# Kernel tuning notes

Hardware: AMD Instinct MI355X
Metric: run time of the kernel (lower is better)

Reference implementation:

```python
import jax, jax.numpy as jnp
import numpy as np

N, T, D, H = 6144, 3072, 128, 4
ALPHA = 0.2
NEG = -9e15


def mhgat(x, mask, W, a_src, a_dst, fc_W, fc_b):
    # x: [n, D], mask: [n, n] (0/1), W: [H, D, D], a_src/a_dst: [H, D]
    Wh = jnp.einsum('nd,hde->hne', x, W)                      # [H, n, D]
    f_s = jnp.einsum('hne,he->hn', Wh, a_src)                 # [H, n]
    f_d = jnp.einsum('hne,he->hn', Wh, a_dst)                 # [H, n]
    e = jax.nn.leaky_relu(f_s[:, :, None] + f_d[:, None, :], ALPHA)  # [H, n, n]
    scores = jnp.where(mask[None, :, :] > 0, e, NEG)
    attn = jax.nn.softmax(scores, axis=-1)                    # masked softmax over neighbors
    h = jnp.einsum('hnm,hme->hne', attn, Wh)                  # [H, n, D]
    h = jax.nn.elu(h)                                         # concat=True -> elu per head
    h = jnp.transpose(h, (1, 0, 2)).reshape(x.shape[0], H * h.shape[-1])  # [n, H*D]
    return jax.nn.relu(h @ fc_W + fc_b)                       # fully_connectedLyer = Linear+ReLU


def setup_inputs() -> dict:
    key = jax.random.key(0)
    ks = jax.random.split(key, 20)
    s = 0.05
    return {
        'x': jax.random.normal(ks[0], (N, D), jnp.float32),
        'adj': jax.random.randint(ks[1], (N, N), 0, 2, jnp.int32),
        't_x': jax.random.normal(ks[2], (T, D), jnp.float32),
        't_adj': jax.random.randint(ks[3], (T, T), 0, 2, jnp.int32),
        'tfidf_x': jax.random.uniform(ks[4], (T, N), jnp.float32),
        # concept-graph MHGAT params
        'Wg': jax.random.normal(ks[5], (H, D, D), jnp.float32) * s,
        'ag_src': jax.random.normal(ks[6], (H, D), jnp.float32) * s,
        'ag_dst': jax.random.normal(ks[7], (H, D), jnp.float32) * s,
        'fcg_W': jax.random.normal(ks[8], (H * D, D), jnp.float32) * s,
        'fcg_b': jnp.zeros((D,), jnp.float32),
        # text-graph MHGAT params
        'Wt': jax.random.normal(ks[9], (H, D, D), jnp.float32) * s,
        'at_src': jax.random.normal(ks[10], (H, D), jnp.float32) * s,
        'at_dst': jax.random.normal(ks[11], (H, D), jnp.float32) * s,
        'fct_W': jax.random.normal(ks[12], (H * D, D), jnp.float32) * s,
        'fct_b': jnp.zeros((D,), jnp.float32),
        # fusion fc params
        'fus_W': jax.random.normal(ks[13], (D, D), jnp.float32) * s,
        'fus_b': jnp.zeros((D,), jnp.float32),
    }


def reference(x, adj, t_x, t_adj, tfidf_x,
              Wg, ag_src, ag_dst, fcg_W, fcg_b,
              Wt, at_src, at_dst, fct_W, fct_b,
              fus_W, fus_b):
    concept = mhgat(x, adj, Wg, ag_src, ag_dst, fcg_W, fcg_b)        # [N, D]
    gat_text = mhgat(t_x, t_adj, Wt, at_src, at_dst, fct_W, fct_b)   # [T, D]
    c_text = tfidf_x.T @ gat_text                                    # [N, D]
    z = jax.nn.sigmoid(concept + c_text)
    fusion = z * concept + (1.0 - z) * c_text
    return jax.nn.relu(fusion @ fus_W + fus_b)
```

## Files before the change

kernel.cpp:

```cpp
#include <hip/hip_runtime.h>
#include <hip/hip_bf16.h>
#include <stdint.h>

#define N_  6144
#define T_  3072
#define D_  128
#define H_  4
#define HD_ 512

typedef float f32x4 __attribute__((ext_vector_type(4)));
typedef short s16x8 __attribute__((ext_vector_type(8)));
typedef _Float16 h16x4 __attribute__((ext_vector_type(4)));

#define GLL16(g, s) __builtin_amdgcn_global_load_lds( \
    (const __attribute__((address_space(1))) unsigned int*)(g), \
    (__attribute__((address_space(3))) unsigned int*)(s), 16, 0, 0)

static __device__ __forceinline__ short f2bf(float f) {
  union { __hip_bfloat16 b; short s; } u;
  u.b = __float2bfloat16(f);
  return u.s;
}

__global__ __launch_bounds__(256) void bits2_kernel(const int* __restrict__ a0,
                                                    const int* __restrict__ a1,
                                                    unsigned long long* __restrict__ b0,
                                                    unsigned long long* __restrict__ b1,
                                                    int nw0, int nw1) {
  int lane = threadIdx.x & 63;
  int gw = (blockIdx.x * blockDim.x + threadIdx.x) >> 6;
  int nw = (gridDim.x * blockDim.x) >> 6;
  int total = nw0 + nw1;
  for (int w = gw; w < total; w += nw) {
    const int* src; unsigned long long* dst; long wi;
    if (w < nw0) { src = a0; dst = b0; wi = w; }
    else         { src = a1; dst = b1; wi = w - nw0; }
    int v = src[wi * 64 + lane];
    unsigned long long b = __ballot(v != 0);
    if (lane == 0) dst[wi] = b;
  }
}

__global__ __launch_bounds__(256) void cvt2_kernel(const float* __restrict__ in0,
                                                   short* __restrict__ out0,
                                                   const float* __restrict__ in1,
                                                   short* __restrict__ out1,
                                                   int c0, int c1) {
  int i = blockIdx.x * blockDim.x + threadIdx.x;
  const float* in; short* out; long ii;
  if (i < c0) { in = in0; out = out0; ii = i; }
  else if (i < c0 + c1) { in = in1; out = out1; ii = i - c0; }
  else return;
  float4 v = *(const float4*)(in + ii * 4);
  short4 o;
  o.x = f2bf(v.x); o.y = f2bf(v.y); o.z = f2bf(v.z); o.w = f2bf(v.w);
  *(short4*)(out + ii * 4) = o;
}

__global__ __launch_bounds__(256) void tcvt2_kernel(const float* __restrict__ in0,
                                                    short* __restrict__ out0,
                                                    const float* __restrict__ in1,
                                                    short* __restrict__ out1,
                                                    int R, int C, long sIn, long sOut,
                                                    int zsplit) {
  __shared__ float t[32][33];
  const float* in; short* out;
  int z = blockIdx.z;
  if (z < zsplit) { in = in0 + (long)z * sIn; out = out0 + (long)z * sOut; }
  else            { in = in1 + (long)(z - zsplit) * sIn; out = out1 + (long)(z - zsplit) * sOut; }
  int c0 = blockIdx.x * 32, r0 = blockIdx.y * 32;
  int tx = threadIdx.x, ty = threadIdx.y;
#pragma unroll
  for (int i = 0; i < 4; ++i)
    t[ty + 8 * i][tx] = in[(long)(r0 + ty + 8 * i) * C + c0 + tx];
  __syncthreads();
#pragma unroll
  for (int i = 0; i < 4; ++i)
    out[(long)(c0 + ty + 8 * i) * R + r0 + tx] = f2bf(t[tx][ty + 8 * i]);
}

__global__ __launch_bounds__(256) void fvec_kernel(const float* __restrict__ x,
                                                   const float* __restrict__ W,
                                                   const float* __restrict__ a_s,
                                                   const float* __restrict__ a_d,
                                                   float* __restrict__ fsA,
                                                   float* __restrict__ fdA,
                                                   int n) {
  __shared__ float usl[128], udl[128], asl[128], adl[128];
  long idx = (long)blockIdx.x * 256 + threadIdx.x;
  int h = (int)(idx / n), i = (int)(idx % n);
  int tid = threadIdx.x;
  if (tid < 128) {
    asl[tid] = a_s[h * D_ + tid];
    adl[tid] = a_d[h * D_ + tid];
  }
  __syncthreads();
  {
    int d = tid & 127;
    const float* wr = W + ((long)h * D_ + d) * D_;
    const float* av = (tid < 128) ? asl : adl;
    float s = 0.f;
#pragma unroll 8
    for (int e = 0; e < D_; ++e) s += wr[e] * av[e];
    if (tid < 128) usl[d] = s; else udl[d] = s;
  }
  __syncthreads();
  const float4* xr = (const float4*)(x + (long)i * D_);
  float s = 0.f, t = 0.f;
#pragma unroll 8
  for (int e4 = 0; e4 < 32; ++e4) {
    float4 xv = xr[e4];
    s += xv.x * usl[4 * e4] + xv.y * usl[4 * e4 + 1] + xv.z * usl[4 * e4 + 2] + xv.w * usl[4 * e4 + 3];
    t += xv.x * udl[4 * e4] + xv.y * udl[4 * e4 + 1] + xv.z * udl[4 * e4 + 2] + xv.w * udl[4 * e4 + 3];
  }
  const float L2E = 1.4426950408889634f;
  fsA[idx] = s * L2E;
  fdA[idx] = t * L2E;
}

__global__ __launch_bounds__(256) void gemm_kernel(const short* __restrict__ A,
                                                   const short* __restrict__ BT,
                                                   int K, int lda, int ldb,
                                                   float* __restrict__ outF, short* __restrict__ outB,
                                                   int ldo, int epi,
                                                   long sA, long sBT, long sOut) {
  int bz = blockIdx.z;
  A += bz * sA;
  BT += bz * sBT;
  __shared__ __align__(16) short bs[2][4096];
  int tid = threadIdx.x, w = tid >> 6, l = tid & 63, lm = l & 15, lg = l >> 4;
  int row0 = blockIdx.x * 64 + w * 16;
  int col0 = blockIdx.y * 128;
  const short* arow = A + (long)(row0 + lm) * lda + 8 * lg;
  const short* bsrc = BT + (long)(col0 + 16 * (2 * w) + lm) * ldb + 8 * lg;
  f32x4 acc[8] = {};
  int nt = K / 32;
  s16x8 af = *(const s16x8*)(arow);
  GLL16(bsrc, &bs[0][(2 * w) * 512]);
  GLL16(bsrc + 16 * ldb, &bs[0][(2 * w + 1) * 512]);
  for (int kt = 0; kt < nt; ++kt) {
    int cur = kt & 1, nxt = cur ^ 1;
    int kb = (kt + 1 < nt ? kt + 1 : kt) * 32;
    s16x8 an = *(const s16x8*)(arow + kb);
    asm volatile("s_waitcnt vmcnt(1)" ::: "memory");
    __builtin_amdgcn_sched_barrier(0);
    __builtin_amdgcn_s_barrier();
    __builtin_amdgcn_sched_barrier(0);
#pragma unroll
    for (int f = 0; f < 8; ++f) {
      s16x8 bf = *(const s16x8*)(&bs[cur][f * 512 + l * 8]);
      acc[f] = __builtin_amdgcn_mfma_f32_16x16x32_bf16(af, bf, acc[f], 0, 0, 0);
    }
    if (kt + 1 < nt) {
      GLL16(bsrc + kb, &bs[nxt][(2 * w) * 512]);
      GLL16(bsrc + kb + 16 * ldb, &bs[nxt][(2 * w + 1) * 512]);
    }
    __builtin_amdgcn_sched_barrier(0);
    af = an;
  }
#pragma unroll
  for (int f = 0; f < 8; ++f) {
    int col = col0 + 16 * f + lm;
#pragma unroll
    for (int r = 0; r < 4; ++r) {
      int row = row0 + 4 * lg + r;
      if (epi == 0) outB[bz * sOut + (long)row * ldo + col] = f2bf(acc[f][r]);
      else          outF[bz * sOut + (long)row * ldo + col] = acc[f][r];
    }
  }
}

__global__ __launch_bounds__(256) void reduce_kernel(const float* __restrict__ P,
                                                     int S, long sP,
                                                     const float* __restrict__ bias,
                                                     short* __restrict__ outB,
                                                     int ldo) {
  __shared__ short sm[128][68];
  int tid = threadIdx.x;
  int r0 = blockIdx.x * 64;
#pragma unroll
  for (int k = 0; k < 8; ++k) {
    int e = tid * 4 + k * 1024;
    int row = e >> 7, col = e & 127;
    f32x4 v = {};
    for (int s = 0; s < S; ++s)
      v += *(const f32x4*)(P + (long)s * sP + (long)(r0 + row) * 128 + col);
    const float4 bv = *(const float4*)(bias + col);
    v[0] += bv.x; v[1] += bv.y; v[2] += bv.z; v[3] += bv.w;
#pragma unroll
    for (int q = 0; q < 4; ++q) v[q] = v[q] > 0.f ? v[q] : 0.f;
    sm[col + 0][row] = f2bf(v[0]);
    sm[col + 1][row] = f2bf(v[1]);
    sm[col + 2][row] = f2bf(v[2]);
    sm[col + 3][row] = f2bf(v[3]);
  }
  __syncthreads();
  int d = tid >> 1, seg = tid & 1;
  short* dst = outB + (long)d * ldo + r0 + seg * 32;
#pragma unroll
  for (int q = 0; q < 8; ++q) {
    short4 o;
    o.x = sm[d][seg * 32 + 4 * q + 0];
    o.y = sm[d][seg * 32 + 4 * q + 1];
    o.z = sm[d][seg * 32 + 4 * q + 2];
    o.w = sm[d][seg * 32 + 4 * q + 3];
    *(short4*)(dst + 4 * q) = o;
  }
}

__global__ __launch_bounds__(256) void attn_kernel(const short* __restrict__ WhT,
                                                   const unsigned char* __restrict__ bits,
                                                   const float* __restrict__ fsA,
                                                   const float* __restrict__ fdA,
                                                   _Float16* __restrict__ pacc,
                                                   float* __restrict__ pz,
                                                   int n, int S) {
  int h = blockIdx.y, sp = blockIdx.z;
  int RB = gridDim.x;
  int klen = n / S, k0 = sp * klen;
  const short* whT = WhT + (long)h * D_ * n;
  const float* fa = fdA + (long)h * n;
  __shared__ __align__(16) short bs[2][4096];
  int tid = threadIdx.x, w = tid >> 6, l = tid & 63, lm = l & 15, lg = l >> 4;
  int i0 = blockIdx.x * 128;
  int r0 = i0 + 32 * w + lm;
  int r1 = r0 + 16;
  float fs0 = fsA[(long)h * n + r0];
  float fs1 = fsA[(long)h * n + r1];
  const unsigned char* brow0 = bits + (long)r0 * (n >> 3);
  const unsigned char* brow1 = bits + (long)r1 * (n >> 3);
  const short* bsrc = whT + (long)(16 * (2 * w) + lm) * n + 8 * lg + k0;
  f32x4 acc0[8] = {}, acc1[8] = {};
  f32x4 az0 = {}, az1 = {};
  s16x8 ones;
#pragma unroll
  for (int j = 0; j < 8; ++j) ones[j] = (short)0x3F80;
  const int NEGB = __float_as_int(-1e30f);
  int nt = klen / 32;
  float favA[8], favB[8];
  unsigned m0A, m1A, m0B, m1B;
  *(float4*)(favA)     = *(const float4*)(fa + k0 + 8 * lg);
  *(float4*)(favA + 4) = *(const float4*)(fa + k0 + 8 * lg + 4);
  m0A = (*(const unsigned*)(brow0 + (k0 >> 3))) >> (8 * lg);
  m1A = (*(const unsigned*)(brow1 + (k0 >> 3))) >> (8 * lg);
  GLL16(bsrc, &bs[0][(2 * w) * 512]);
  GLL16(bsrc + 16 * n, &bs[0][(2 * w + 1) * 512]);

#define ATTN_STEP(KT, FAVC, M0C, M1C, FAVN, M0N, M1N)                           \
  {                                                                             \
    int cur = (KT) & 1, nxt = cur ^ 1;                                          \
    int kb = ((KT) + 1 < nt ? (KT) + 1 : (KT)) * 32;                            \
    *(float4*)(FAVN)     = *(const float4*)(fa + k0 + kb + 8 * lg);             \
    *(float4*)(FAVN + 4) = *(const float4*)(fa + k0 + kb + 8 * lg + 4);         \
    M0N = (*(const unsigned*)(brow0 + ((k0 + kb) >> 3))) >> (8 * lg);           \
    M1N = (*(const unsigned*)(brow1 + ((k0 + kb) >> 3))) >> (8 * lg);           \
    union { s16x8 v; unsigned u[4]; } af0, af1;                                 \
    _Pragma("unroll")                                                           \
    for (int jj = 0; jj < 4; ++jj) {                                            \
      float xa = FAVC[2 * jj], xb2 = FAVC[2 * jj + 1];                          \
      int ta = ((int)(M0C << (31 - 2 * jj))) >> 31;                             \
      int tb = ((int)(M0C << (30 - 2 * jj))) >> 31;                             \
      float ua = fs0 + xa, ub = fs0 + xb2;                                      \
      ua = __int_as_float((ta & __float_as_int(ua)) | (~ta & NEGB));            \
      ub = __int_as_float((tb & __float_as_int(ub)) | (~tb & NEGB));            \
      float pa = __builtin_amdgcn_exp2f(fmaxf(ua, 0.2f * ua));                  \
      float pb = __builtin_amdgcn_exp2f(fmaxf(ub, 0.2f * ub));                  \
      af0.u[jj] = __builtin_amdgcn_perm(__float_as_uint(pb) + 0x8000u,          \
                                        __float_as_uint(pa) + 0x8000u, 0x07060302); \
      ta = ((int)(M1C << (31 - 2 * jj))) >> 31;                                 \
      tb = ((int)(M1C << (30 - 2 * jj))) >> 31;                                 \
      ua = fs1 + xa; ub = fs1 + xb2;                                            \
      ua = __int_as_float((ta & __float_as_int(ua)) | (~ta & NEGB));            \
      ub = __int_as_float((tb & __float_as_int(ub)) | (~tb & NEGB));            \
      pa = __builtin_amdgcn_exp2f(fmaxf(ua, 0.2f * ua));                        \
      pb = __builtin_amdgcn_exp2f(fmaxf(ub, 0.2f * ub));                        \
      af1.u[jj] = __builtin_amdgcn_perm(__float_as_uint(pb) + 0x8000u,          \
                                        __float_as_uint(pa) + 0x8000u, 0x07060302); \
    }                                                                           \
    asm volatile("s_waitcnt vmcnt(4)" ::: "memory");                            \
    __builtin_amdgcn_sched_barrier(0);                                          \
    __builtin_amdgcn_s_barrier();                                               \
    __builtin_amdgcn_sched_barrier(0);                                          \
    _Pragma("unroll")                                                           \
    for (int f = 0; f < 8; ++f) {                                               \
      s16x8 bf = *(const s16x8*)(&bs[cur][f * 512 + l * 8]);                    \
      acc0[f] = __builtin_amdgcn_mfma_f32_16x16x32_bf16(af0.v, bf, acc0[f], 0, 0, 0); \
      acc1[f] = __builtin_amdgcn_mfma_f32_16x16x32_bf16(af1.v, bf, acc1[f], 0, 0, 0); \
    }                                                                           \
    az0 = __builtin_amdgcn_mfma_f32_16x16x32_bf16(af0.v, ones, az0, 0, 0, 0);   \
    az1 = __builtin_amdgcn_mfma_f32_16x16x32_bf16(af1.v, ones, az1, 0, 0, 0);   \
    if ((KT) + 1 < nt) {                                                        \
      GLL16(bsrc + kb, &bs[nxt][(2 * w) * 512]);                                \
      GLL16(bsrc + kb + 16 * n, &bs[nxt][(2 * w + 1) * 512]);                   \
    }                                                                           \
    __builtin_amdgcn_sched_barrier(0);                                          \
  }

  for (int kt = 0; kt < nt; kt += 2) {
    ATTN_STEP(kt,     favA, m0A, m1A, favB, m0B, m1B);
    ATTN_STEP(kt + 1, favB, m0B, m1B, favA, m0A, m1A);
  }
#undef ATTN_STEP

  long base = (long)(h * RB + blockIdx.x) * S + sp;
  if (lm == 0) {
#pragma unroll
    for (int r = 0; r < 4; ++r) {
      pz[base * 128 + 32 * w + 4 * lg + r] = az0[r];
      pz[base * 128 + 32 * w + 16 + 4 * lg + r] = az1[r];
    }
  }
  long pb = base * 16384;
#pragma unroll
  for (int f = 0; f < 8; ++f)
#pragma unroll
    for (int r = 0; r < 4; ++r) {
      pacc[pb + (long)(32 * w + 4 * lg + r) * 128 + 16 * f + lm] = (_Float16)acc0[f][r];
      pacc[pb + (long)(32 * w + 16 + 4 * lg + r) * 128 + 16 * f + lm] = (_Float16)acc1[f][r];
    }
}

__global__ __launch_bounds__(256) void attn_combine_kernel(const _Float16* __restrict__ pacc,
                                                           const float* __restrict__ pz,
                                                           short* __restrict__ hcat,
                                                           int S) {
  int h = blockIdx.y, rb = blockIdx.x;
  int RB = gridDim.x;
  long base = (long)(h * RB + rb) * S;
  __shared__ float zl[128];
  int tid = threadIdx.x;
  if (tid < 128) {
    float zv = 0.f;
    for (int s = 0; s < S; ++s) zv += pz[(base + s) * 128 + tid];
    zl[tid] = 1.f / zv;
  }
  __syncthreads();
  int i0 = rb * 128;
#pragma unroll
  for (int k = 0; k < 16; ++k) {
    int e = tid * 4 + k * 1024;
    int row = e >> 7, col = e & 127;
    f32x4 v = {};
    for (int s = 0; s < S; ++s) {
      h16x4 hv = *(const h16x4*)(pacc + (base + s) * 16384 + e);
      v[0] += (float)hv[0]; v[1] += (float)hv[1];
      v[2] += (float)hv[2]; v[3] += (float)hv[3];
    }
    float iz = zl[row];
    short4 o;
    float t;
    t = v[0] * iz; o.x = f2bf(t > 0.f ? t : __expf(t) - 1.f);
    t = v[1] * iz; o.y = f2bf(t > 0.f ? t : __expf(t) - 1.f);
    t = v[2] * iz; o.z = f2bf(t > 0.f ? t : __expf(t) - 1.f);
    t = v[3] * iz; o.w = f2bf(t > 0.f ? t : __expf(t) - 1.f);
    *(short4*)(hcat + (long)(i0 + row) * HD_ + h * D_ + col) = o;
  }
}

__global__ __launch_bounds__(256) void fusion_kernel(const float* __restrict__ fcPg,
                                                     int Sf, long sPg,
                                                     const float* __restrict__ fcg_b,
                                                     const float* __restrict__ ctextP,
                                                     int Sc, long sCt,
                                                     const short* __restrict__ fusT,
                                                     const float* __restrict__ fus_b,
                                                     float* __restrict__ out) {
  __shared__ __align__(16) short als[64 * 136];
  int tid = threadIdx.x;
  int r0 = blockIdx.x * 64;
#pragma unroll
  for (int it = 0; it < 8; ++it) {
    int e = it * 1024 + tid * 4;
    int r = e >> 7, c = e & 127;
    f32x4 cv = {};
    for (int s = 0; s < Sf; ++s)
      cv += *(const f32x4*)(fcPg + (long)s * sPg + (long)(r0 + r) * D_ + c);
    const float4 bv = *(const float4*)(fcg_b + c);
    cv[0] += bv.x; cv[1] += bv.y; cv[2] += bv.z; cv[3] += bv.w;
#pragma unroll
    for (int q = 0; q < 4; ++q) cv[q] = cv[q] > 0.f ? cv[q] : 0.f;
    f32x4 tv = {};
    for (int s = 0; s < Sc; ++s)
      tv += *(const f32x4*)(ctextP + (long)s * sCt + (long)(r0 + r) * D_ + c);
    short4 o;
    {
      float s0 = cv[0] + tv[0]; float z = 1.f / (1.f + __expf(-s0)); o.x = f2bf(tv[0] + z * (cv[0] - tv[0]));
      s0 = cv[1] + tv[1]; z = 1.f / (1.f + __expf(-s0)); o.y = f2bf(tv[1] + z * (cv[1] - tv[1]));
      s0 = cv[2] + tv[2]; z = 1.f / (1.f + __expf(-s0)); o.z = f2bf(tv[2] + z * (cv[2] - tv[2]));
      s0 = cv[3] + tv[3]; z = 1.f / (1.f + __expf(-s0)); o.w = f2bf(tv[3] + z * (cv[3] - tv[3]));
    }
    *(short4*)(als + (long)r * 136 + c) = o;
  }
  __syncthreads();
  int w = tid >> 6, l = tid & 63, lm = l & 15, lg = l >> 4;
  f32x4 acc[8] = {};
#pragma unroll
  for (int kt = 0; kt < 4; ++kt) {
    int kb = kt * 32;
    s16x8 af = *(const s16x8*)(als + (16 * w + lm) * 136 + kb + 8 * lg);
#pragma unroll
    for (int f = 0; f < 8; ++f) {
      s16x8 bf = *(const s16x8*)(fusT + (long)(16 * f + lm) * D_ + kb + 8 * lg);
      acc[f] = __builtin_amdgcn_mfma_f32_16x16x32_bf16(af, bf, acc[f], 0, 0, 0);
    }
  }
#pragma unroll
  for (int f = 0; f < 8; ++f) {
    int col = 16 * f + lm;
#pragma unroll
    for (int r = 0; r < 4; ++r) {
      float v = acc[f][r] + fus_b[col];
      v = v > 0.f ? v : 0.f;
      out[(long)(r0 + 16 * w + 4 * lg + r) * D_ + col] = v;
    }
  }
}

extern "C" void kernel_launch(void* const* d_in, const int* in_sizes, int n_in,
                              void* d_out, int out_size, void* d_ws, size_t ws_size,
                              hipStream_t stream) {
  (void)in_sizes; (void)n_in; (void)out_size;
  const float* x      = (const float*)d_in[0];
  const int*   adj    = (const int*)d_in[1];
  const float* t_x    = (const float*)d_in[2];
  const int*   t_adj  = (const int*)d_in[3];
  const float* tfidf  = (const float*)d_in[4];
  const float* Wg     = (const float*)d_in[5];
  const float* ag_src = (const float*)d_in[6];
  const float* ag_dst = (const float*)d_in[7];
  const float* fcg_W  = (const float*)d_in[8];
  const float* fcg_b  = (const float*)d_in[9];
  const float* Wt     = (const float*)d_in[10];
  const float* at_src = (const float*)d_in[11];
  const float* at_dst = (const float*)d_in[12];
  const float* fct_W  = (const float*)d_in[13];
  const float* fct_b  = (const float*)d_in[14];
  const float* fus_W  = (const float*)d_in[15];
  const float* fus_b  = (const float*)d_in[16];
  float* out = (float*)d_out;

  char* ws = (char*)d_ws;
  size_t off = 0;
  auto alloc = [&](size_t bytes) -> char* {
    char* p = ws + off;
    off = (off + bytes + 255) & ~(size_t)255;
    return p;
  };
  unsigned long long* bitsG = (unsigned long long*)alloc((size_t)N_ * N_ / 8);
  unsigned long long* bitsT = (unsigned long long*)alloc((size_t)T_ * T_ / 8);
  short* xb     = (short*)alloc((size_t)N_ * D_ * 2);
  short* txb    = (short*)alloc((size_t)T_ * D_ * 2);
  short* WgT    = (short*)alloc((size_t)H_ * D_ * D_ * 2);
  short* WtT    = (short*)alloc((size_t)H_ * D_ * D_ * 2);
  short* fcgT   = (short*)alloc((size_t)HD_ * D_ * 2);
  short* fctT   = (short*)alloc((size_t)HD_ * D_ * 2);
  short* fusT   = (short*)alloc((size_t)D_ * D_ * 2);
  short* tfidfT = (short*)alloc((size_t)N_ * T_ * 2);
  short* WhTg   = (short*)alloc((size_t)H_ * D_ * N_ * 2);
  short* WhTt   = (short*)alloc((size_t)H_ * D_ * T_ * 2);
  float* fsAg = (float*)alloc((size_t)H_ * N_ * 4);
  float* fdAg = (float*)alloc((size_t)H_ * N_ * 4);
  float* fsAt = (float*)alloc((size_t)H_ * T_ * 4);
  float* fdAt = (float*)alloc((size_t)H_ * T_ * 4);
  short* hcatG = (short*)alloc((size_t)N_ * HD_ * 2);
  short* hcatT = (short*)alloc((size_t)T_ * HD_ * 2);
  short* gatT  = (short*)alloc((size_t)D_ * T_ * 2);

  const int RBg = N_ / 128, RBt = T_ / 128;
  const size_t paccG1 = (size_t)H_ * RBg * 16384 * 2;
  const size_t paccT1 = (size_t)H_ * RBt * 16384 * 2;
  const size_t pzG1   = (size_t)H_ * RBg * 128 * 4;
  const size_t pzT1   = (size_t)H_ * RBt * 128 * 4;
  const size_t fcPg1  = (size_t)N_ * D_ * 4;
  const size_t fcPt1  = (size_t)T_ * D_ * 4;
  const size_t ctp1   = (size_t)N_ * D_ * 4;
  size_t rem = (ws_size > off + (1 << 20)) ? (ws_size - off - (1 << 20)) : 0;
  int Sg = 2, St = 2, Sf = 1, Sc = 1;
  size_t needFull = 8 * (paccG1 + pzG1) + 8 * (paccT1 + pzT1) + 4 * fcPg1 + 4 * fcPt1 + 4 * ctp1;
  size_t needMid  = 4 * (paccG1 + pzG1) + 4 * (paccT1 + pzT1) + 2 * fcPg1 + 2 * fcPt1 + 2 * ctp1;
  if (rem >= needFull)      { Sg = 8; St = 8; Sf = 4; Sc = 4; }
  else if (rem >= needMid)  { Sg = 4; St = 4; Sf = 2; Sc = 2; }
  _Float16* paccG = (_Float16*)alloc(Sg * paccG1);
  float* pzG   = (float*)alloc(Sg * pzG1);
  _Float16* paccT = (_Float16*)alloc(St * paccT1);
  float* pzT   = (float*)alloc(St * pzT1);
  float* fcPg  = (float*)alloc(Sf * fcPg1);
  float* fcPt  = (float*)alloc(Sf * fcPt1);
  float* ctextP = (float*)alloc(Sc * ctp1);

  bits2_kernel<<<dim3(1536), dim3(256), 0, stream>>>(adj, t_adj, bitsG, bitsT,
                                                     N_ * N_ / 64, T_ * T_ / 64);
  cvt2_kernel<<<dim3((N_ + T_) * D_ / 1024), dim3(256), 0, stream>>>(
      x, xb, t_x, txb, N_ * D_ / 4, T_ * D_ / 4);
  tcvt2_kernel<<<dim3(4, 4, 8), dim3(32, 8), 0, stream>>>(
      Wg, WgT, Wt, WtT, D_, D_, (long)D_ * D_, (long)D_ * D_, 4);
  tcvt2_kernel<<<dim3(4, 16, 2), dim3(32, 8), 0, stream>>>(
      fcg_W, fcgT, fct_W, fctT, HD_, D_, 0, 0, 1);
  tcvt2_kernel<<<dim3(4, 4, 1), dim3(32, 8), 0, stream>>>(
      fus_W, fusT, fus_W, fusT, D_, D_, 0, 0, 1);
  tcvt2_kernel<<<dim3(N_ / 32, T_ / 32, 1), dim3(32, 8), 0, stream>>>(
      tfidf, tfidfT, tfidf, tfidfT, T_, N_, 0, 0, 1);
  fvec_kernel<<<dim3(H_ * N_ / 256), dim3(256), 0, stream>>>(x, Wg, ag_src, ag_dst, fsAg, fdAg, N_);
  fvec_kernel<<<dim3(H_ * T_ / 256), dim3(256), 0, stream>>>(t_x, Wt, at_src, at_dst, fsAt, fdAt, T_);

  gemm_kernel<<<dim3(2, N_ / 128, H_), dim3(256), 0, stream>>>(
      WgT, xb, D_, D_, D_, nullptr, WhTg, N_, 0, (long)D_ * D_, 0, (long)D_ * N_);
  gemm_kernel<<<dim3(2, T_ / 128, H_), dim3(256), 0, stream>>>(
      WtT, txb, D_, D_, D_, nullptr, WhTt, T_, 0, (long)D_ * D_, 0, (long)D_ * T_);

  attn_kernel<<<dim3(RBg, H_, Sg), dim3(256), 0, stream>>>(
      WhTg, (const unsigned char*)bitsG, fsAg, fdAg, paccG, pzG, N_, Sg);
  attn_combine_kernel<<<dim3(RBg, H_), dim3(256), 0, stream>>>(paccG, pzG, hcatG, Sg);
  attn_kernel<<<dim3(RBt, H_, St), dim3(256), 0, stream>>>(
      WhTt, (const unsigned char*)bitsT, fsAt, fdAt, paccT, pzT, T_, St);
  attn_combine_kernel<<<dim3(RBt, H_), dim3(256), 0, stream>>>(paccT, pzT, hcatT, St);

  gemm_kernel<<<dim3(N_ / 64, 1, Sf), dim3(256), 0, stream>>>(
      hcatG, fcgT, HD_ / Sf, HD_, HD_, fcPg, nullptr, D_, 3,
      (long)(HD_ / Sf), (long)(HD_ / Sf), (long)N_ * D_);
  gemm_kernel<<<dim3(T_ / 64, 1, Sf), dim3(256), 0, stream>>>(
      hcatT, fctT, HD_ / Sf, HD_, HD_, fcPt, nullptr, D_, 3,
      (long)(HD_ / Sf), (long)(HD_ / Sf), (long)T_ * D_);
  reduce_kernel<<<dim3(T_ / 64), dim3(256), 0, stream>>>(
      fcPt, Sf, (long)T_ * D_, fct_b, gatT, T_);

  gemm_kernel<<<dim3(N_ / 64, 1, Sc), dim3(256), 0, stream>>>(
      tfidfT, gatT, T_ / Sc, T_, T_, ctextP, nullptr, D_, 3,
      (long)(T_ / Sc), (long)(T_ / Sc), (long)N_ * D_);

  fusion_kernel<<<dim3(N_ / 64), dim3(256), 0, stream>>>(
      fcPg, Sf, (long)N_ * D_, fcg_b, ctextP, Sc, (long)N_ * D_, fusT, fus_b, out);
}
```

Measured before the change: 414.0 us.

## Factor attention exponentials into per-node precomputed terms and batch mask bit packing

```diff
diff --git a/kernel.cpp b/kernel.cpp
--- a/kernel.cpp
+++ b/kernel.cpp
@@ -22,7 +22,7 @@
   return u.s;
 }
 
-__global__ __launch_bounds__(256) void bits2_kernel(const int* __restrict__ a0,
+__global__ __launch_bounds__(256) void bits8_kernel(const int* __restrict__ a0,
                                                     const int* __restrict__ a1,
                                                     unsigned long long* __restrict__ b0,
                                                     unsigned long long* __restrict__ b1,
@@ -30,14 +30,26 @@
   int lane = threadIdx.x & 63;
   int gw = (blockIdx.x * blockDim.x + threadIdx.x) >> 6;
   int nw = (gridDim.x * blockDim.x) >> 6;
-  int total = nw0 + nw1;
-  for (int w = gw; w < total; w += nw) {
+  int total8 = (nw0 + nw1) >> 3;
+  for (int g = gw; g < total8; g += nw) {
+    int w = g * 8;
     const int* src; unsigned long long* dst; long wi;
     if (w < nw0) { src = a0; dst = b0; wi = w; }
     else         { src = a1; dst = b1; wi = w - nw0; }
-    int v = src[wi * 64 + lane];
-    unsigned long long b = __ballot(v != 0);
-    if (lane == 0) dst[wi] = b;
+    int v[8];
+#pragma unroll
+    for (int j = 0; j < 8; ++j) v[j] = src[(wi + j) * 64 + lane];
+    unsigned long long bb[8];
+#pragma unroll
+    for (int j = 0; j < 8; ++j) bb[j] = __ballot(v[j] != 0);
+    if (lane == 0) {
+      ulonglong2 s01 = {bb[0], bb[1]}, s23 = {bb[2], bb[3]};
+      ulonglong2 s45 = {bb[4], bb[5]}, s67 = {bb[6], bb[7]};
+      *(ulonglong2*)(dst + wi + 0) = s01;
+      *(ulonglong2*)(dst + wi + 2) = s23;
+      *(ulonglong2*)(dst + wi + 4) = s45;
+      *(ulonglong2*)(dst + wi + 6) = s67;
+    }
   }
 }
 
@@ -83,8 +95,9 @@
                                                    const float* __restrict__ W,
                                                    const float* __restrict__ a_s,
                                                    const float* __restrict__ a_d,
-                                                   float* __restrict__ fsA,
-                                                   float* __restrict__ fdA,
+                                                   float* __restrict__ ea, float* __restrict__ ec,
+                                                   float* __restrict__ inv,
+                                                   float* __restrict__ eb, float* __restrict__ ed,
                                                    int n) {
   __shared__ float usl[128], udl[128], asl[128], adl[128];
   long idx = (long)blockIdx.x * 256 + threadIdx.x;
@@ -114,8 +127,12 @@
     t += xv.x * udl[4 * e4] + xv.y * udl[4 * e4 + 1] + xv.z * udl[4 * e4 + 2] + xv.w * udl[4 * e4 + 3];
   }
   const float L2E = 1.4426950408889634f;
-  fsA[idx] = s * L2E;
-  fdA[idx] = t * L2E;
+  float fs = s * L2E, fd = t * L2E;
+  ea[idx]  = exp2f(fs);
+  ec[idx]  = exp2f(0.2f * fs);
+  inv[idx] = exp2f(-fs);
+  eb[idx]  = exp2f(fd);
+  ed[idx]  = exp2f(0.2f * fd);
 }
 
 __global__ __launch_bounds__(256) void gemm_kernel(const short* __restrict__ A,
@@ -210,8 +227,11 @@
 
 __global__ __launch_bounds__(256) void attn_kernel(const short* __restrict__ WhT,
                                                    const unsigned char* __restrict__ bits,
-                                                   const float* __restrict__ fsA,
-                                                   const float* __restrict__ fdA,
+                                                   const float* __restrict__ eaA,
+                                                   const float* __restrict__ ecA,
+                                                   const float* __restrict__ invA,
+                                                   const float* __restrict__ ebA,
+                                                   const float* __restrict__ edA,
                                                    _Float16* __restrict__ pacc,
                                                    float* __restrict__ pz,
                                                    int n, int S) {
@@ -219,14 +239,16 @@
   int RB = gridDim.x;
   int klen = n / S, k0 = sp * klen;
   const short* whT = WhT + (long)h * D_ * n;
-  const float* fa = fdA + (long)h * n;
+  const float* ebp = ebA + (long)h * n;
+  const float* edp = edA + (long)h * n;
   __shared__ __align__(16) short bs[2][4096];
   int tid = threadIdx.x, w = tid >> 6, l = tid & 63, lm = l & 15, lg = l >> 4;
   int i0 = blockIdx.x * 128;
   int r0 = i0 + 32 * w + lm;
   int r1 = r0 + 16;
-  float fs0 = fsA[(long)h * n + r0];
-  float fs1 = fsA[(long)h * n + r1];
+  float ea0 = eaA[(long)h * n + r0], ea1 = eaA[(long)h * n + r1];
+  float ec0 = ecA[(long)h * n + r0], ec1 = ecA[(long)h * n + r1];
+  float iv0 = invA[(long)h * n + r0], iv1 = invA[(long)h * n + r1];
   const unsigned char* brow0 = bits + (long)r0 * (n >> 3);
   const unsigned char* brow1 = bits + (long)r1 * (n >> 3);
   const short* bsrc = whT + (long)(16 * (2 * w) + lm) * n + 8 * lg + k0;
@@ -235,49 +257,53 @@
   s16x8 ones;
 #pragma unroll
   for (int j = 0; j < 8; ++j) ones[j] = (short)0x3F80;
-  const int NEGB = __float_as_int(-1e30f);
   int nt = klen / 32;
-  float favA[8], favB[8];
+  float ebR[8], edR[8], ebS[8], edS[8];
   unsigned m0A, m1A, m0B, m1B;
-  *(float4*)(favA)     = *(const float4*)(fa + k0 + 8 * lg);
-  *(float4*)(favA + 4) = *(const float4*)(fa + k0 + 8 * lg + 4);
+  *(float4*)(ebR)     = *(const float4*)(ebp + k0 + 8 * lg);
+  *(float4*)(ebR + 4) = *(const float4*)(ebp + k0 + 8 * lg + 4);
+  *(float4*)(edR)     = *(const float4*)(edp + k0 + 8 * lg);
+  *(float4*)(edR + 4) = *(const float4*)(edp + k0 + 8 * lg + 4);
   m0A = (*(const unsigned*)(brow0 + (k0 >> 3))) >> (8 * lg);
   m1A = (*(const unsigned*)(brow1 + (k0 >> 3))) >> (8 * lg);
   GLL16(bsrc, &bs[0][(2 * w) * 512]);
   GLL16(bsrc + 16 * n, &bs[0][(2 * w + 1) * 512]);
 
-#define ATTN_STEP(KT, FAVC, M0C, M1C, FAVN, M0N, M1N)                           \
+#define ATTN_STEP(KT, EBC, EDC, M0C, M1C, EBN, EDN, M0N, M1N)                   \
   {                                                                             \
     int cur = (KT) & 1, nxt = cur ^ 1;                                          \
     int kb = ((KT) + 1 < nt ? (KT) + 1 : (KT)) * 32;                            \
-    *(float4*)(FAVN)     = *(const float4*)(fa + k0 + kb + 8 * lg);             \
-    *(float4*)(FAVN + 4) = *(const float4*)(fa + k0 + kb + 8 * lg + 4);         \
+    *(float4*)(EBN)     = *(const float4*)(ebp + k0 + kb + 8 * lg);             \
+    *(float4*)(EBN + 4) = *(const float4*)(ebp + k0 + kb + 8 * lg + 4);         \
+    *(float4*)(EDN)     = *(const float4*)(edp + k0 + kb + 8 * lg);             \
+    *(float4*)(EDN + 4) = *(const float4*)(edp + k0 + kb + 8 * lg + 4);         \
     M0N = (*(const unsigned*)(brow0 + ((k0 + kb) >> 3))) >> (8 * lg);           \
     M1N = (*(const unsigned*)(brow1 + ((k0 + kb) >> 3))) >> (8 * lg);           \
     union { s16x8 v; unsigned u[4]; } af0, af1;                                 \
     _Pragma("unroll")                                                           \
     for (int jj = 0; jj < 4; ++jj) {                                            \
-      float xa = FAVC[2 * jj], xb2 = FAVC[2 * jj + 1];                          \
+      float bva = EBC[2 * jj], bvb = EBC[2 * jj + 1];                           \
+      float dva = EDC[2 * jj], dvb = EDC[2 * jj + 1];                           \
       int ta = ((int)(M0C << (31 - 2 * jj))) >> 31;                             \
       int tb = ((int)(M0C << (30 - 2 * jj))) >> 31;                             \
-      float ua = fs0 + xa, ub = fs0 + xb2;                                      \
-      ua = __int_as_float((ta & __float_as_int(ua)) | (~ta & NEGB));            \
-      ub = __int_as_float((tb & __float_as_int(ub)) | (~tb & NEGB));            \
-      float pa = __builtin_amdgcn_exp2f(fmaxf(ua, 0.2f * ua));                  \
-      float pb = __builtin_amdgcn_exp2f(fmaxf(ub, 0.2f * ub));                  \
+      bool ca = bva > iv0, cb = bvb > iv0;                                      \
+      float pa = (ca ? bva : dva) * (ca ? ea0 : ec0);                           \
+      float pb = (cb ? bvb : dvb) * (cb ? ea0 : ec0);                           \
+      pa = __int_as_float(ta & __float_as_int(pa));                             \
+      pb = __int_as_float(tb & __float_as_int(pb));                             \
       af0.u[jj] = __builtin_amdgcn_perm(__float_as_uint(pb) + 0x8000u,          \
                                         __float_as_uint(pa) + 0x8000u, 0x07060302); \
       ta = ((int)(M1C << (31 - 2 * jj))) >> 31;                                 \
       tb = ((int)(M1C << (30 - 2 * jj))) >> 31;                                 \
-      ua = fs1 + xa; ub = fs1 + xb2;                                            \
-      ua = __int_as_float((ta & __float_as_int(ua)) | (~ta & NEGB));            \
-      ub = __int_as_float((tb & __float_as_int(ub)) | (~tb & NEGB));            \
-      pa = __builtin_amdgcn_exp2f(fmaxf(ua, 0.2f * ua));                        \
-      pb = __builtin_amdgcn_exp2f(fmaxf(ub, 0.2f * ub));                        \
+      ca = bva > iv1; cb = bvb > iv1;                                           \
+      pa = (ca ? bva : dva) * (ca ? ea1 : ec1);                                 \
+      pb = (cb ? bvb : dvb) * (cb ? ea1 : ec1);                                 \
+      pa = __int_as_float(ta & __float_as_int(pa));                             \
+      pb = __int_as_float(tb & __float_as_int(pb));                             \
       af1.u[jj] = __builtin_amdgcn_perm(__float_as_uint(pb) + 0x8000u,          \
                                         __float_as_uint(pa) + 0x8000u, 0x07060302); \
     }                                                                           \
-    asm volatile("s_waitcnt vmcnt(4)" ::: "memory");                            \
+    asm volatile("s_waitcnt vmcnt(6)" ::: "memory");                            \
     __builtin_amdgcn_sched_barrier(0);                                          \
     __builtin_amdgcn_s_barrier();                                               \
     __builtin_amdgcn_sched_barrier(0);                                          \
@@ -297,8 +323,8 @@
   }
 
   for (int kt = 0; kt < nt; kt += 2) {
-    ATTN_STEP(kt,     favA, m0A, m1A, favB, m0B, m1B);
-    ATTN_STEP(kt + 1, favB, m0B, m1B, favA, m0A, m1A);
+    ATTN_STEP(kt,     ebR, edR, m0A, m1A, ebS, edS, m0B, m1B);
+    ATTN_STEP(kt + 1, ebS, edS, m0B, m1B, ebR, edR, m0A, m1A);
   }
 #undef ATTN_STEP
 
@@ -458,10 +484,16 @@
   short* tfidfT = (short*)alloc((size_t)N_ * T_ * 2);
   short* WhTg   = (short*)alloc((size_t)H_ * D_ * N_ * 2);
   short* WhTt   = (short*)alloc((size_t)H_ * D_ * T_ * 2);
-  float* fsAg = (float*)alloc((size_t)H_ * N_ * 4);
-  float* fdAg = (float*)alloc((size_t)H_ * N_ * 4);
-  float* fsAt = (float*)alloc((size_t)H_ * T_ * 4);
-  float* fdAt = (float*)alloc((size_t)H_ * T_ * 4);
+  float* eaG  = (float*)alloc((size_t)H_ * N_ * 4);
+  float* ecG  = (float*)alloc((size_t)H_ * N_ * 4);
+  float* invG = (float*)alloc((size_t)H_ * N_ * 4);
+  float* ebG  = (float*)alloc((size_t)H_ * N_ * 4);
+  float* edG  = (float*)alloc((size_t)H_ * N_ * 4);
+  float* eaT  = (float*)alloc((size_t)H_ * T_ * 4);
+  float* ecT  = (float*)alloc((size_t)H_ * T_ * 4);
+  float* invT = (float*)alloc((size_t)H_ * T_ * 4);
+  float* ebT  = (float*)alloc((size_t)H_ * T_ * 4);
+  float* edT  = (float*)alloc((size_t)H_ * T_ * 4);
   short* hcatG = (short*)alloc((size_t)N_ * HD_ * 2);
   short* hcatT = (short*)alloc((size_t)T_ * HD_ * 2);
   short* gatT  = (short*)alloc((size_t)D_ * T_ * 2);
@@ -488,7 +520,7 @@
   float* fcPt  = (float*)alloc(Sf * fcPt1);
   float* ctextP = (float*)alloc(Sc * ctp1);
 
-  bits2_kernel<<<dim3(1536), dim3(256), 0, stream>>>(adj, t_adj, bitsG, bitsT,
+  bits8_kernel<<<dim3(1536), dim3(256), 0, stream>>>(adj, t_adj, bitsG, bitsT,
                                                      N_ * N_ / 64, T_ * T_ / 64);
   cvt2_kernel<<<dim3((N_ + T_) * D_ / 1024), dim3(256), 0, stream>>>(
       x, xb, t_x, txb, N_ * D_ / 4, T_ * D_ / 4);
@@ -500,8 +532,10 @@
       fus_W, fusT, fus_W, fusT, D_, D_, 0, 0, 1);
   tcvt2_kernel<<<dim3(N_ / 32, T_ / 32, 1), dim3(32, 8), 0, stream>>>(
       tfidf, tfidfT, tfidf, tfidfT, T_, N_, 0, 0, 1);
-  fvec_kernel<<<dim3(H_ * N_ / 256), dim3(256), 0, stream>>>(x, Wg, ag_src, ag_dst, fsAg, fdAg, N_);
-  fvec_kernel<<<dim3(H_ * T_ / 256), dim3(256), 0, stream>>>(t_x, Wt, at_src, at_dst, fsAt, fdAt, T_);
+  fvec_kernel<<<dim3(H_ * N_ / 256), dim3(256), 0, stream>>>(
+      x, Wg, ag_src, ag_dst, eaG, ecG, invG, ebG, edG, N_);
+  fvec_kernel<<<dim3(H_ * T_ / 256), dim3(256), 0, stream>>>(
+      t_x, Wt, at_src, at_dst, eaT, ecT, invT, ebT, edT, T_);
 
   gemm_kernel<<<dim3(2, N_ / 128, H_), dim3(256), 0, stream>>>(
       WgT, xb, D_, D_, D_, nullptr, WhTg, N_, 0, (long)D_ * D_, 0, (long)D_ * N_);
@@ -509,10 +543,10 @@
       WtT, txb, D_, D_, D_, nullptr, WhTt, T_, 0, (long)D_ * D_, 0, (long)D_ * T_);
 
   attn_kernel<<<dim3(RBg, H_, Sg), dim3(256), 0, stream>>>(
-      WhTg, (const unsigned char*)bitsG, fsAg, fdAg, paccG, pzG, N_, Sg);
+      WhTg, (const unsigned char*)bitsG, eaG, ecG, invG, ebG, edG, paccG, pzG, N_, Sg);
   attn_combine_kernel<<<dim3(RBg, H_), dim3(256), 0, stream>>>(paccG, pzG, hcatG, Sg);
   attn_kernel<<<dim3(RBt, H_, St), dim3(256), 0, stream>>>(
-      WhTt, (const unsigned char*)bitsT, fsAt, fdAt, paccT, pzT, T_, St);
+      WhTt, (const unsigned char*)bitsT, eaT, ecT, invT, ebT, edT, paccT, pzT, T_, St);
   attn_combine_kernel<<<dim3(RBt, H_), dim3(256), 0, stream>>>(paccT, pzT, hcatT, St);
 
   gemm_kernel<<<dim3(N_ / 64, 1, Sf), dim3(256), 0, stream>>>(
```

Result: faster. 392.4 us (-5.2%).
